# Optimization experiments

Measured on AMD Instinct MI355X. Metric: run time of the kernel, lower is better.

Reference implementation:

```python
import jax, jax.numpy as jnp
import numpy as np

B, C_IN, T = 32, 22, 5000
EMB, P = 64, 100
HOP, NFFT, SR = 25, 128, 250
MIN_SZ, MAX_SZ = 10, 100
OC = 40
SCALES = (9, 25, 49)
FC = OC * len(SCALES)
_freqs = np.arange(NFFT // 2 + 1) * SR / NFFT
MU_IDX = np.nonzero((_freqs >= 8) & (_freqs <= 13))[0]   # bins 5,6
BETA_IDX = np.nonzero((_freqs >= 13) & (_freqs <= 30))[0]  # bins 7..15


def setup_inputs() -> dict:
    key = jax.random.key(0)
    k = iter(jax.random.split(key, 16))
    inp = {"x": jax.random.normal(next(k), (B, C_IN, T), jnp.float32)}
    for i, s in enumerate(SCALES):
        inp[f"ms{i}_w1"] = jax.random.normal(next(k), (OC, 1, 1, s), jnp.float32) * 0.05
        inp[f"ms{i}_b1"] = jnp.zeros((OC,), jnp.float32)
        inp[f"ms{i}_w2"] = jax.random.normal(next(k), (OC, OC, C_IN, 1), jnp.float32) * 0.05
        inp[f"ms{i}_b2"] = jnp.zeros((OC,), jnp.float32)
        inp[f"ms{i}_g"] = jnp.ones((OC,), jnp.float32)
        inp[f"ms{i}_bt"] = jnp.zeros((OC,), jnp.float32)
        inp[f"ms{i}_m"] = jnp.zeros((OC,), jnp.float32)
        inp[f"ms{i}_v"] = jnp.ones((OC,), jnp.float32)
    inp["a_w1"] = jax.random.normal(next(k), (C_IN // 2, C_IN, 3), jnp.float32) * 0.05
    inp["a_b1"] = jnp.zeros((C_IN // 2,), jnp.float32)
    inp["a_g"] = jnp.ones((C_IN // 2,), jnp.float32)
    inp["a_bt"] = jnp.zeros((C_IN // 2,), jnp.float32)
    inp["a_m"] = jnp.zeros((C_IN // 2,), jnp.float32)
    inp["a_v"] = jnp.ones((C_IN // 2,), jnp.float32)
    inp["a_w2"] = jax.random.normal(next(k), (1, C_IN // 2, 1), jnp.float32) * 0.05
    inp["a_b2"] = jnp.zeros((1,), jnp.float32)
    inp["proj_w"] = jax.random.normal(next(k), (EMB, FC, 1), jnp.float32) * 0.05
    inp["proj_b"] = jnp.zeros((EMB,), jnp.float32)
    return inp


def _conv1d(x, w, pad):
    return jax.lax.conv_general_dilated(x, w, (1,), [(pad, pad)],
                                        dimension_numbers=("NCH", "OIH", "NCH"))


def _bn(y, g, bt, m, v):  # eval-mode BatchNorm over channel dim of [B, C, T]
    return (y - m[None, :, None]) * jax.lax.rsqrt(v[None, :, None] + 1e-5) * g[None, :, None] + bt[None, :, None]


def _branch(x, w1, b1, w2, b2, g, bt, m, v):
    # Conv2d(1,OC,(1,ks)) on [B,1,C,T] == per-channel 1D conv over time.
    oc, _, _, ks = w1.shape
    b_, c_, t_ = x.shape
    y = _conv1d(x.reshape(b_ * c_, 1, t_), w1.reshape(oc, 1, ks), (ks - 1) // 2) + b1[None, :, None]
    y = y.reshape(b_, c_, oc, t_).transpose(0, 2, 1, 3)            # [B, OC, C, T]
    # Conv2d(OC,OC,(C,1)) collapses the channel (height) dim.
    y = jnp.einsum("oih,biht->bot", w2[..., 0], y) + b2[None, :, None]
    return jax.nn.elu(_bn(y, g, bt, m, v))                         # [B, OC, T]


def _stft_power(x):
    # torchaudio Spectrogram: center=True, reflect pad, periodic hann, power=2
    pad = NFFT // 2
    xp = jnp.pad(x, ((0, 0), (0, 0), (pad, pad)), mode="reflect")
    nfr = T // HOP  # module truncates to t // hop frames
    idx = jnp.arange(nfr)[:, None] * HOP + jnp.arange(NFFT)[None, :]
    win = 0.5 * (1.0 - jnp.cos(2.0 * jnp.pi * jnp.arange(NFFT) / NFFT))
    frames = xp[..., idx] * win                                    # [B, C, nfr, NFFT]
    spec = jnp.fft.rfft(frames, axis=-1)
    return spec.real ** 2 + spec.imag ** 2                         # [B, C, nfr, NFFT//2+1]


def _interp_linear(a, n):  # F.interpolate(mode='linear', align_corners=False) on [B, L]
    L = a.shape[-1]
    pos = jnp.clip((jnp.arange(n) + 0.5) * (L / n) - 0.5, 0.0, L - 1.0)
    lo = jnp.floor(pos).astype(jnp.int32)
    hi = jnp.minimum(lo + 1, L - 1)
    w = pos - lo
    return a[:, lo] * (1.0 - w) + a[:, hi] * w


def _adaptive_grid(act):
    w = 1.0 / (act + 1e-6)
    w = w / jnp.sum(w, axis=1, keepdims=True)
    gs = jnp.clip(w * T, MIN_SZ, MAX_SZ)
    gs = gs * (T / jnp.sum(gs, axis=1, keepdims=True))
    gsr = jnp.round(gs).astype(jnp.int32)
    gsr = gsr.at[:, -1].add(T - jnp.sum(gsr, axis=1))
    gsf = jnp.clip(gsr, MIN_SZ, MAX_SZ)
    gsf = gsf.at[:, -1].add(T - jnp.sum(gsf, axis=1))
    return jnp.where(gsf < MIN_SZ, MIN_SZ, gsf)


def _forward(x, ms0_w1, ms0_b1, ms0_w2, ms0_b2, ms0_g, ms0_bt, ms0_m, ms0_v,
             ms1_w1, ms1_b1, ms1_w2, ms1_b2, ms1_g, ms1_bt, ms1_m, ms1_v,
             ms2_w1, ms2_b1, ms2_w2, ms2_b2, ms2_g, ms2_bt, ms2_m, ms2_v,
             a_w1, a_b1, a_g, a_bt, a_m, a_v, a_w2, a_b2, proj_w, proj_b):
    # ---- frequency-domain activity detector ----
    spec = _stft_power(x)                                          # [B, C, 200, F]
    comb = spec[..., MU_IDX].mean(-1) + spec[..., BETA_IDX].mean(-1)  # [B, C, 200]
    a = jax.nn.relu(_bn(_conv1d(comb, a_w1, 1) + a_b1[None, :, None], a_g, a_bt, a_m, a_v))
    a = jnp.einsum("oi,bit->bot", a_w2[..., 0], a)[:, 0] + a_b2[0]
    activity = jax.nn.sigmoid(a)                                   # [B, 200]
    act_i = _interp_linear(activity, P)                            # [B, P]
    grid = _adaptive_grid(act_i)                                   # [B, P] int32, sums ~= T
    ends = jnp.cumsum(grid, axis=1)
    starts = ends - grid
    # ---- multi-scale CNN features ----
    feats = jnp.concatenate([
        _branch(x, ms0_w1, ms0_b1, ms0_w2, ms0_b2, ms0_g, ms0_bt, ms0_m, ms0_v),
        _branch(x, ms1_w1, ms1_b1, ms1_w2, ms1_b2, ms1_g, ms1_bt, ms1_m, ms1_v),
        _branch(x, ms2_w1, ms2_b1, ms2_w2, ms2_b2, ms2_g, ms2_bt, ms2_m, ms2_v)],
        axis=1)                                                    # [B, FC, T]
    # ---- ragged per-patch avg+max pooling via segment reductions ----
    tix = jnp.arange(T)
    seg = jax.vmap(lambda e: jnp.searchsorted(e, tix, side="right"))(ends)  # [B,T] in [0,P]
    flat = (seg + jnp.arange(B)[:, None] * (P + 1)).reshape(-1)
    f = feats.transpose(0, 2, 1).reshape(B * T, FC)
    nseg = B * (P + 1)  # extra slot collects any overflow timesteps
    sums = jax.ops.segment_sum(f, flat, num_segments=nseg)
    cnt = jax.ops.segment_sum(jnp.ones((B * T, 1), f.dtype), flat, num_segments=nseg)
    mx = jax.ops.segment_max(f, flat, num_segments=nseg)
    avg = sums / jnp.maximum(cnt, 1.0)
    mx = jnp.where(cnt > 0, mx, 0.0)
    pooled = (avg + mx).reshape(B, P + 1, FC)[:, :P]               # combined avg+max
    valid = ((ends <= T) & (starts < ends))[..., None]
    pooled = jnp.where(valid, pooled, 0.0)
    emb = jnp.einsum("oc,bpc->bpo", proj_w[..., 0], pooled) + proj_b  # [B, P, EMB]
    return emb, grid, act_i


def reference(x, ms0_w1, ms0_b1, ms0_w2, ms0_b2, ms0_g, ms0_bt, ms0_m, ms0_v,
              ms1_w1, ms1_b1, ms1_w2, ms1_b2, ms1_g, ms1_bt, ms1_m, ms1_v,
              ms2_w1, ms2_b1, ms2_w2, ms2_b2, ms2_g, ms2_bt, ms2_m, ms2_v,
              a_w1, a_b1, a_g, a_bt, a_m, a_v, a_w2, a_b2, proj_w, proj_b):
    return _forward(x, ms0_w1, ms0_b1, ms0_w2, ms0_b2, ms0_g, ms0_bt, ms0_m, ms0_v,
                    ms1_w1, ms1_b1, ms1_w2, ms1_b2, ms1_g, ms1_bt, ms1_m, ms1_v,
                    ms2_w1, ms2_b1, ms2_w2, ms2_b2, ms2_g, ms2_bt, ms2_m, ms2_v,
                    a_w1, a_b1, a_g, a_bt, a_m, a_v, a_w2, a_b2, proj_w, proj_b)
```

## Files before the change

kernel.cpp:

```cpp
#include <hip/hip_runtime.h>
#include <hip/hip_bf16.h>
#include <hip/hip_fp8.h>
#include <math.h>
#include <string.h>

#define B 32
#define CIN 22
#define T 5000
#define EMB 64
#define P 100
#define HOP 25
#define OC 40
#define FC 120
#define NBIN 11
#define NFR 200

#define TCH 256
#define CROWS 304
#define RS8 40

#define XPAD 5128
#define TWROW 24

typedef __attribute__((ext_vector_type(4))) float f32x4;

__device__ __forceinline__ unsigned short f2bf(float f) {
  unsigned u = __float_as_uint(f);
  unsigned r = (u + 0x7FFFu + ((u >> 16) & 1u)) >> 16;
  return (unsigned short)r;
}
__device__ __forceinline__ float bf2f(unsigned short u) {
  return __uint_as_float(((unsigned)u) << 16);
}
__device__ __forceinline__ unsigned char f2fp8(float f) {
  __hip_fp8_e4m3 q(f);
  return (unsigned char)q.__x;
}
__device__ __forceinline__ float fast_elu(float y) {
  return y > 0.f ? y : (__builtin_amdgcn_exp2f(y * 1.44269504088896340736f) - 1.0f);
}
__device__ __forceinline__ unsigned pack2bf(float a, float b) {
  __hip_bfloat162 h = __float22bfloat162_rn(make_float2(a, b));
  unsigned u;
  memcpy(&u, &h, 4);
  return u;
}
__device__ __forceinline__ float wave_sum_f(float v) {
  #pragma unroll
  for (int off = 1; off < 64; off <<= 1) v += __shfl_xor(v, off);
  return v;
}
__device__ __forceinline__ int wave_sum_i(int v) {
  #pragma unroll
  for (int off = 1; off < 64; off <<= 1) v += __shfl_xor(v, off);
  return v;
}

struct SetupArgs {
  const float* w1[3]; const float* b1[3]; const float* w2[3]; const float* b2[3];
  const float* g[3];  const float* bt[3]; const float* m[3];  const float* v[3];
  unsigned char* pw8;
  float* A; float* Bc; float* tw;
};

__global__ __launch_bounds__(256) void setup_all(SetupArgs args) {
  int bx = blockIdx.x;
  int tid = threadIdx.x;
  if (bx < 63) {
    int id = bx * 256 + tid;
    if (id < 15936) {
      int fi = id >> 6;
      int lane = id & 63;
      int s, KS, fl;
      if (fi < 27)       { s = 0; KS = 9;  fl = fi; }
      else if (fi < 102) { s = 1; KS = 25; fl = fi - 27; }
      else               { s = 2; KS = 49; fl = fi - 102; }
      int k = fl / 3, ot = fl - k * 3;
      int m = lane & 15, hb = (lane >> 4) << 3;
      int o = ot * 16 + m;
      float val[8];
      #pragma unroll
      for (int j = 0; j < 8; ++j) val[j] = 0.f;
      if (o < OC && hb < CIN) {
        const float* w1 = args.w1[s];
        const float* w2 = args.w2[s];
        if (hb + 8 <= CIN) {
          for (int i = 0; i < OC; ++i) {
            float wv = w1[i * KS + k];
            const float* w2r = w2 + (size_t)(o * OC + i) * CIN + hb;
            float2 a0 = *(const float2*)(w2r + 0);
            float2 a1 = *(const float2*)(w2r + 2);
            float2 a2 = *(const float2*)(w2r + 4);
            float2 a3 = *(const float2*)(w2r + 6);
            val[0] = fmaf(a0.x, wv, val[0]); val[1] = fmaf(a0.y, wv, val[1]);
            val[2] = fmaf(a1.x, wv, val[2]); val[3] = fmaf(a1.y, wv, val[3]);
            val[4] = fmaf(a2.x, wv, val[4]); val[5] = fmaf(a2.y, wv, val[5]);
            val[6] = fmaf(a3.x, wv, val[6]); val[7] = fmaf(a3.y, wv, val[7]);
          }
        } else {
          for (int i = 0; i < OC; ++i) {
            float wv = w1[i * KS + k];
            const float* w2r = w2 + (size_t)(o * OC + i) * CIN + hb;
            float2 a0 = *(const float2*)(w2r + 0);
            float2 a1 = *(const float2*)(w2r + 2);
            float2 a2 = *(const float2*)(w2r + 4);
            val[0] = fmaf(a0.x, wv, val[0]); val[1] = fmaf(a0.y, wv, val[1]);
            val[2] = fmaf(a1.x, wv, val[2]); val[3] = fmaf(a1.y, wv, val[3]);
            val[4] = fmaf(a2.x, wv, val[4]); val[5] = fmaf(a2.y, wv, val[5]);
          }
        }
      }
      unsigned char bytes[8];
      #pragma unroll
      for (int j = 0; j < 8; ++j) bytes[j] = f2fp8(val[j]);
      long long pk;
      memcpy(&pk, bytes, 8);
      *(long long*)(args.pw8 + (size_t)fi * 512 + lane * 8) = pk;
    }
  } else if (bx < 69) {
    int id = (bx - 63) * 256 + tid;
    if (id < 1408) {
      int n = id & 127, k = id >> 7;
      const double PI = 3.14159265358979323846;
      double ang = -2.0 * PI * (double)((k + 5) * n) / 128.0;
      double win = 0.5 * (1.0 - cos(2.0 * PI * (double)n / 128.0));
      args.tw[n * TWROW + 2 * k]     = (float)(cos(ang) * win);
      args.tw[n * TWROW + 2 * k + 1] = (float)(sin(ang) * win);
    } else if (id < 1536) {
      int n = id - 1408;
      args.tw[n * TWROW + 22] = 0.f;
      args.tw[n * TWROW + 23] = 0.f;
    }
  } else {
    if (tid < 120) {
      int s = tid / 40, o = tid - s * 40;
      const float* w2 = args.w2[s];
      float sc = args.g[s][o] / sqrtf(args.v[s][o] + 1e-5f);
      float cc = args.b2[s][o];
      for (int i = 0; i < OC; ++i) {
        float sh = 0.f;
        for (int h = 0; h < CIN; ++h) sh += w2[(o * OC + i) * CIN + h];
        cc = fmaf(args.b1[s][i], sh, cc);
      }
      args.A[tid] = sc;
      args.Bc[tid] = cc * sc + (args.bt[s][o] - args.m[s][o] * sc);
    }
  }
}

__global__ __launch_bounds__(256) void stft_comb(const float* __restrict__ x,
                                                 const float* __restrict__ tw,
                                                 float* __restrict__ comb) {
  __shared__ float xsh[XPAD];
  int bc = blockIdx.x;
  const float* xr = x + (size_t)bc * T;
  int tid = threadIdx.x;
  for (int i = tid; i < XPAD; i += 256) {
    int mm = i - 64;
    mm = (mm < 0) ? -mm : mm;
    mm = (mm >= T) ? (2 * T - 2 - mm) : mm;
    xsh[i] = xr[mm];
  }
  __syncthreads();
  int fr = tid;
  if (fr < NFR) {
    float cr[NBIN], ci[NBIN];
    #pragma unroll
    for (int k = 0; k < NBIN; ++k) { cr[k] = 0.f; ci[k] = 0.f; }
    const float* xw = xsh + fr * HOP;
    #pragma unroll 2
    for (int n = 0; n < 128; ++n) {
      float xv = xw[n];
      const float4* t4 = reinterpret_cast<const float4*>(tw + n * TWROW);
      float4 w0 = t4[0], w1 = t4[1], w2 = t4[2], w3 = t4[3], w4 = t4[4], w5 = t4[5];
      cr[0] = fmaf(xv, w0.x, cr[0]); ci[0] = fmaf(xv, w0.y, ci[0]);
      cr[1] = fmaf(xv, w0.z, cr[1]); ci[1] = fmaf(xv, w0.w, ci[1]);
      cr[2] = fmaf(xv, w1.x, cr[2]); ci[2] = fmaf(xv, w1.y, ci[2]);
      cr[3] = fmaf(xv, w1.z, cr[3]); ci[3] = fmaf(xv, w1.w, ci[3]);
      cr[4] = fmaf(xv, w2.x, cr[4]); ci[4] = fmaf(xv, w2.y, ci[4]);
      cr[5] = fmaf(xv, w2.z, cr[5]); ci[5] = fmaf(xv, w2.w, ci[5]);
      cr[6] = fmaf(xv, w3.x, cr[6]); ci[6] = fmaf(xv, w3.y, ci[6]);
      cr[7] = fmaf(xv, w3.z, cr[7]); ci[7] = fmaf(xv, w3.w, ci[7]);
      cr[8] = fmaf(xv, w4.x, cr[8]); ci[8] = fmaf(xv, w4.y, ci[8]);
      cr[9] = fmaf(xv, w4.z, cr[9]); ci[9] = fmaf(xv, w4.w, ci[9]);
      cr[10] = fmaf(xv, w5.x, cr[10]); ci[10] = fmaf(xv, w5.y, ci[10]);
    }
    float p[NBIN];
    #pragma unroll
    for (int k = 0; k < NBIN; ++k) p[k] = cr[k] * cr[k] + ci[k] * ci[k];
    float beta = 0.f;
    #pragma unroll
    for (int k = 2; k < NBIN; ++k) beta += p[k];
    comb[bc * NFR + fr] = 0.5f * (p[0] + p[1]) + beta * (1.f / 9.f);
  }
}

struct MidSmem {
  union {
    struct {
      float cl[CIN * NFR];
      float actL[NFR];
      float aiL[P];
      float fL[P];
      int giL[P];
      int sI[P];
      float red;
    } a;
    unsigned char xs8[CROWS * RS8];
  };
};

template <int KS, int FB, int SBASE>
__device__ __forceinline__ void scale_body(const unsigned char* __restrict__ xs8,
                                           const unsigned char* __restrict__ pw8,
                                           const float* __restrict__ Aff,
                                           const float* __restrict__ Bff,
                                           unsigned short* __restrict__ feats,
                                           int b, int t0, int wt0, int lane) {
  constexpr int PAD = (KS - 1) / 2;
  const int n = lane & 15, q = lane >> 4;
  f32x4 acc[3][2];
  #pragma unroll
  for (int ot = 0; ot < 3; ++ot)
    #pragma unroll
    for (int ti = 0; ti < 2; ++ti)
      acc[ot][ti] = (f32x4){0.f, 0.f, 0.f, 0.f};

  const unsigned char* pws = pw8 + (size_t)FB * 512 + lane * 8;
  long long A0 = *(const long long*)(pws);
  long long A1 = *(const long long*)(pws + 512);
  long long A2 = *(const long long*)(pws + 1024);
  #pragma unroll 1
  for (int k = 0; k < KS; ++k) {
    long long nA0 = 0, nA1 = 0, nA2 = 0;
    if (k + 1 < KS) {
      const unsigned char* p = pws + (size_t)(k + 1) * 3 * 512;
      nA0 = *(const long long*)(p);
      nA1 = *(const long long*)(p + 512);
      nA2 = *(const long long*)(p + 1024);
    }
    int rbase = 24 - PAD + k + wt0 + n;
    #pragma unroll
    for (int ti = 0; ti < 2; ++ti) {
      long long Bf = *(const long long*)(xs8 + (rbase + ti * 16) * RS8 + q * 8);
      acc[0][ti] = __builtin_amdgcn_mfma_f32_16x16x32_fp8_fp8(A0, Bf, acc[0][ti], 0, 0, 0);
      acc[1][ti] = __builtin_amdgcn_mfma_f32_16x16x32_fp8_fp8(A1, Bf, acc[1][ti], 0, 0, 0);
      acc[2][ti] = __builtin_amdgcn_mfma_f32_16x16x32_fp8_fp8(A2, Bf, acc[2][ti], 0, 0, 0);
    }
    A0 = nA0; A1 = nA1; A2 = nA2;
  }
  #pragma unroll
  for (int ot = 0; ot < 3; ++ot) {
    int obase = ot * 16 + q * 4;
    if (obase < OC) {
      float Av0 = Aff[SBASE + obase + 0], Bv0 = Bff[SBASE + obase + 0];
      float Av1 = Aff[SBASE + obase + 1], Bv1 = Bff[SBASE + obase + 1];
      float Av2 = Aff[SBASE + obase + 2], Bv2 = Bff[SBASE + obase + 2];
      float Av3 = Aff[SBASE + obase + 3], Bv3 = Bff[SBASE + obase + 3];
      #pragma unroll
      for (int ti = 0; ti < 2; ++ti) {
        int tt = t0 + wt0 + ti * 16 + n;
        if (tt < T) {
          uint2 pk;
          pk.x = pack2bf(fast_elu(fmaf(acc[ot][ti][0], Av0, Bv0)),
                         fast_elu(fmaf(acc[ot][ti][1], Av1, Bv1)));
          pk.y = pack2bf(fast_elu(fmaf(acc[ot][ti][2], Av2, Bv2)),
                         fast_elu(fmaf(acc[ot][ti][3], Av3, Bv3)));
          *reinterpret_cast<uint2*>(feats + (size_t)(b * T + tt) * FC + SBASE + obase) = pk;
        }
      }
    }
  }
}

struct MidArgs {
  const float* x;
  const unsigned char* pw8;
  const float* Aff; const float* Bff;
  unsigned short* feats;
  const float* comb;
  const float* aw1; const float* ab1;
  const float* ag;  const float* abt;
  const float* am;  const float* av;
  const float* aw2; const float* ab2;
  float* out_grid; float* out_acti;
  int* ends_i; int* grid_i;
};

__global__ __launch_bounds__(512) void mid_all(MidArgs args) {
  __shared__ MidSmem sm;
  int bx = blockIdx.x;
  int tid = threadIdx.x;
  if (bx >= B) {
    int cx = bx - B;
    int b = cx / 20, t0 = (cx - b * 20) * TCH;
    for (int i = tid; i < CROWS * RS8 / 4; i += 512)
      reinterpret_cast<unsigned*>(sm.xs8)[i] = 0u;
    __syncthreads();
    for (int idx = tid; idx < CIN * CROWS; idx += 512) {
      int h = idx / CROWS, tl = idx - h * CROWS;
      int gt = t0 - 24 + tl;
      float v = (gt >= 0 && gt < T) ? args.x[(size_t)(b * CIN + h) * T + gt] : 0.f;
      sm.xs8[tl * RS8 + h] = f2fp8(v);
    }
    __syncthreads();
    int wv = tid >> 6, lane = tid & 63;
    int wt0 = wv * 32;
    scale_body<9, 0, 0>(sm.xs8, args.pw8, args.Aff, args.Bff, args.feats, b, t0, wt0, lane);
    scale_body<25, 27, 40>(sm.xs8, args.pw8, args.Aff, args.Bff, args.feats, b, t0, wt0, lane);
    scale_body<49, 102, 80>(sm.xs8, args.pw8, args.Aff, args.Bff, args.feats, b, t0, wt0, lane);
  } else {
    int b = bx;
    for (int i = tid; i < CIN * NFR; i += 512) sm.a.cl[i] = args.comb[b * CIN * NFR + i];
    __syncthreads();
    int t = tid;
    if (t < NFR) {
      float z = args.ab2[0];
      for (int o = 0; o < 11; ++o) {
        float s = args.ab1[o];
        for (int i = 0; i < CIN; ++i) {
          const float* wr = args.aw1 + o * 66 + i * 3;
          const float* crow = sm.a.cl + i * NFR;
          if (t > 0)       s = fmaf(wr[0], crow[t - 1], s);
          s = fmaf(wr[1], crow[t], s);
          if (t < NFR - 1) s = fmaf(wr[2], crow[t + 1], s);
        }
        float rs = 1.0f / sqrtf(args.av[o] + 1e-5f);
        float y = (s - args.am[o]) * rs * args.ag[o] + args.abt[o];
        y = fmaxf(y, 0.f);
        z = fmaf(args.aw2[o], y, z);
      }
      sm.a.actL[t] = 1.f / (1.f + expf(-z));
    }
    __syncthreads();
    if (t < P) {
      float ai = 0.5f * (sm.a.actL[2 * t] + sm.a.actL[2 * t + 1]);
      sm.a.aiL[t] = ai;
      args.out_acti[b * P + t] = ai;
      sm.a.fL[t] = 1.f / (ai + 1e-6f);
    }
    __syncthreads();
    if (t < 64) {
      float v = sm.a.fL[t] + ((t + 64 < P) ? sm.a.fL[t + 64] : 0.f);
      v = wave_sum_f(v);
      if (t == 0) sm.a.red = v;
    }
    __syncthreads();
    float sw = sm.a.red;
    if (t < P) {
      float ggv = (sm.a.fL[t] / sw) * 5000.f;
      ggv = fminf(fmaxf(ggv, 10.f), 100.f);
      sm.a.fL[t] = ggv;
    }
    __syncthreads();
    if (t < 64) {
      float v = sm.a.fL[t] + ((t + 64 < P) ? sm.a.fL[t + 64] : 0.f);
      v = wave_sum_f(v);
      if (t == 0) sm.a.red = v;
    }
    __syncthreads();
    float r = 5000.f / sm.a.red;
    if (t < P) sm.a.giL[t] = (int)rintf(sm.a.fL[t] * r);
    __syncthreads();
    if (t < 64) {
      int v = sm.a.giL[t] + ((t + 64 < P) ? sm.a.giL[t + 64] : 0);
      v = wave_sum_i(v);
      if (t == 0) sm.a.red = __int_as_float(v);
    }
    __syncthreads();
    if (t == P - 1) sm.a.giL[P - 1] += 5000 - __float_as_int(sm.a.red);
    __syncthreads();
    if (t < P) sm.a.giL[t] = min(max(sm.a.giL[t], 10), 100);
    __syncthreads();
    if (t < 64) {
      int v = sm.a.giL[t] + ((t + 64 < P) ? sm.a.giL[t + 64] : 0);
      v = wave_sum_i(v);
      if (t == 0) sm.a.red = __int_as_float(v);
    }
    __syncthreads();
    if (t == P - 1) sm.a.giL[P - 1] += 5000 - __float_as_int(sm.a.red);
    __syncthreads();
    if (t < P) sm.a.sI[t] = max(sm.a.giL[t], 10);
    __syncthreads();
    #pragma unroll
    for (int off = 1; off < P; off <<= 1) {
      int v = 0;
      if (t < P && t >= off) v = sm.a.sI[t - off];
      __syncthreads();
      if (t < P) sm.a.sI[t] += v;
      __syncthreads();
    }
    if (t < P) {
      int g2 = max(sm.a.giL[t], 10);
      args.out_grid[b * P + t] = (float)g2;
      args.grid_i[b * P + t] = g2;
      args.ends_i[b * P + t] = sm.a.sI[t];
    }
  }
}

__global__ __launch_bounds__(256) void pool_proj(const unsigned short* __restrict__ feats,
                                                 const int* __restrict__ ends_i,
                                                 const int* __restrict__ grid_i,
                                                 const float* __restrict__ proj_w,
                                                 const float* __restrict__ proj_b,
                                                 float* __restrict__ out_emb) {
  int bp = blockIdx.x;
  int b = bp / P;
  int end = ends_i[bp];
  int gr = grid_i[bp];
  int start = end - gr;
  __shared__ float lds_s[16 * FC];
  __shared__ float lds_m[16 * FC];
  __shared__ float pooled[FC];
  int tid = threadIdx.x;
  bool valid = (end <= T);
  int g = tid % 15;
  int r = tid / 15;
  if (valid && r < 16) {
    float s[8], m[8];
    #pragma unroll
    for (int j = 0; j < 8; ++j) { s[j] = 0.f; m[j] = -INFINITY; }
    const unsigned short* base = feats + (size_t)(b * T + start) * FC + g * 8;
    for (int i = r; i < gr; i += 16) {
      uint4 u4 = *reinterpret_cast<const uint4*>(base + (size_t)i * FC);
      unsigned w[4] = {u4.x, u4.y, u4.z, u4.w};
      #pragma unroll
      for (int j = 0; j < 4; ++j) {
        float v0 = bf2f((unsigned short)(w[j] & 0xffffu));
        float v1 = bf2f((unsigned short)(w[j] >> 16));
        s[2 * j] += v0; s[2 * j + 1] += v1;
        m[2 * j] = fmaxf(m[2 * j], v0); m[2 * j + 1] = fmaxf(m[2 * j + 1], v1);
      }
    }
    #pragma unroll
    for (int j = 0; j < 8; ++j) {
      lds_s[r * FC + g * 8 + j] = s[j];
      lds_m[r * FC + g * 8 + j] = m[j];
    }
  }
  __syncthreads();
  if (tid < FC) {
    if (valid) {
      float s = 0.f, mx = -INFINITY;
      #pragma unroll
      for (int rr = 0; rr < 16; ++rr) {
        s += lds_s[rr * FC + tid];
        mx = fmaxf(mx, lds_m[rr * FC + tid]);
      }
      pooled[tid] = s / (float)gr + mx;
    } else {
      pooled[tid] = 0.f;
    }
  }
  __syncthreads();
  if (tid < EMB) {
    float e = proj_b[tid];
    const float* wr = proj_w + tid * FC;
    #pragma unroll 8
    for (int c = 0; c < FC; ++c) e = fmaf(wr[c], pooled[c], e);
    out_emb[(size_t)bp * EMB + tid] = e;
  }
}

extern "C" void kernel_launch(void* const* d_in, const int* in_sizes, int n_in,
                              void* d_out, int out_size, void* d_ws, size_t ws_size,
                              hipStream_t stream) {
  const float* x = (const float*)d_in[0];
  const float* aw1 = (const float*)d_in[25];
  const float* ab1 = (const float*)d_in[26];
  const float* ag  = (const float*)d_in[27];
  const float* abt = (const float*)d_in[28];
  const float* am  = (const float*)d_in[29];
  const float* av  = (const float*)d_in[30];
  const float* aw2 = (const float*)d_in[31];
  const float* ab2 = (const float*)d_in[32];
  const float* proj_w = (const float*)d_in[33];
  const float* proj_b = (const float*)d_in[34];

  float* wsf = (float*)d_ws;
  float* A    = wsf;
  float* Bc   = wsf + 120;
  float* tw   = wsf + 240;
  float* comb = wsf + 4096;
  int* ends_i = (int*)(wsf + 144896);
  int* grid_i = (int*)(wsf + 148096);
  unsigned char* pw8 = (unsigned char*)(wsf + 151296);
  unsigned short* feats = (unsigned short*)(wsf + 215040);

  float* out      = (float*)d_out;
  float* out_emb  = out;
  float* out_grid = out + 204800;
  float* out_acti = out + 208000;

  SetupArgs sa;
  MidArgs ma;
  for (int s = 0; s < 3; ++s) {
    sa.w1[s] = (const float*)d_in[1 + 8 * s];
    sa.b1[s] = (const float*)d_in[2 + 8 * s];
    sa.w2[s] = (const float*)d_in[3 + 8 * s];
    sa.b2[s] = (const float*)d_in[4 + 8 * s];
    sa.g[s]  = (const float*)d_in[5 + 8 * s];
    sa.bt[s] = (const float*)d_in[6 + 8 * s];
    sa.m[s]  = (const float*)d_in[7 + 8 * s];
    sa.v[s]  = (const float*)d_in[8 + 8 * s];
  }
  sa.pw8 = pw8; sa.A = A; sa.Bc = Bc; sa.tw = tw;

  ma.x = x; ma.pw8 = pw8; ma.Aff = A; ma.Bff = Bc; ma.feats = feats;
  ma.comb = comb; ma.aw1 = aw1; ma.ab1 = ab1; ma.ag = ag; ma.abt = abt;
  ma.am = am; ma.av = av; ma.aw2 = aw2; ma.ab2 = ab2;
  ma.out_grid = out_grid; ma.out_acti = out_acti;
  ma.ends_i = ends_i; ma.grid_i = grid_i;

  setup_all<<<70, 256, 0, stream>>>(sa);
  stft_comb<<<B * CIN, 256, 0, stream>>>(x, tw, comb);
  mid_all<<<B + 20 * B, 512, 0, stream>>>(ma);
  pool_proj<<<B * P, 256, 0, stream>>>(feats, ends_i, grid_i, proj_w, proj_b, out_emb);
}
```

Before: 262.8 us.

## Widen per-wave time tile to 64 rows and prefetch B fragments in conv MFMA loop

Each wave now accumulates four 16-row time tiles instead of two, and the block shrinks from 512 to 256 threads so a block still covers 256 time steps. Each weight fragment loaded from global memory is therefore reused across twice as many MFMAs. The shared-memory B fragments are also software-prefetched one tap ahead, and the loop is unrolled by two with a peeled final iteration. The cost is more accumulator registers and half as many threads for the shared-memory staging and the attention branch of the same kernel.

```diff
diff --git a/kernel.cpp b/kernel.cpp
--- a/kernel.cpp
+++ b/kernel.cpp
@@ -219,36 +219,61 @@
                                            int b, int t0, int wt0, int lane) {
   constexpr int PAD = (KS - 1) / 2;
   const int n = lane & 15, q = lane >> 4;
-  f32x4 acc[3][2];
+  f32x4 acc[3][4];
   #pragma unroll
   for (int ot = 0; ot < 3; ++ot)
     #pragma unroll
-    for (int ti = 0; ti < 2; ++ti)
+    for (int ti = 0; ti < 4; ++ti)
       acc[ot][ti] = (f32x4){0.f, 0.f, 0.f, 0.f};
 
   const unsigned char* pws = pw8 + (size_t)FB * 512 + lane * 8;
+  const unsigned char* xrow = xs8 + (24 - PAD + wt0 + n) * RS8 + q * 8;
   long long A0 = *(const long long*)(pws);
   long long A1 = *(const long long*)(pws + 512);
   long long A2 = *(const long long*)(pws + 1024);
-  #pragma unroll 1
-  for (int k = 0; k < KS; ++k) {
-    long long nA0 = 0, nA1 = 0, nA2 = 0;
-    if (k + 1 < KS) {
-      const unsigned char* p = pws + (size_t)(k + 1) * 3 * 512;
-      nA0 = *(const long long*)(p);
-      nA1 = *(const long long*)(p + 512);
-      nA2 = *(const long long*)(p + 1024);
-    }
-    int rbase = 24 - PAD + k + wt0 + n;
-    #pragma unroll
-    for (int ti = 0; ti < 2; ++ti) {
-      long long Bf = *(const long long*)(xs8 + (rbase + ti * 16) * RS8 + q * 8);
-      acc[0][ti] = __builtin_amdgcn_mfma_f32_16x16x32_fp8_fp8(A0, Bf, acc[0][ti], 0, 0, 0);
-      acc[1][ti] = __builtin_amdgcn_mfma_f32_16x16x32_fp8_fp8(A1, Bf, acc[1][ti], 0, 0, 0);
-      acc[2][ti] = __builtin_amdgcn_mfma_f32_16x16x32_fp8_fp8(A2, Bf, acc[2][ti], 0, 0, 0);
-    }
+  long long B0 = *(const long long*)(xrow);
+  long long B1 = *(const long long*)(xrow + 16 * RS8);
+  long long B2 = *(const long long*)(xrow + 32 * RS8);
+  long long B3 = *(const long long*)(xrow + 48 * RS8);
+  #pragma unroll 2
+  for (int k = 0; k < KS - 1; ++k) {
+    const unsigned char* p = pws + (size_t)(k + 1) * 1536;
+    long long nA0 = *(const long long*)(p);
+    long long nA1 = *(const long long*)(p + 512);
+    long long nA2 = *(const long long*)(p + 1024);
+    const unsigned char* xr = xrow + (k + 1) * RS8;
+    long long nB0 = *(const long long*)(xr);
+    long long nB1 = *(const long long*)(xr + 16 * RS8);
+    long long nB2 = *(const long long*)(xr + 32 * RS8);
+    long long nB3 = *(const long long*)(xr + 48 * RS8);
+    acc[0][0] = __builtin_amdgcn_mfma_f32_16x16x32_fp8_fp8(A0, B0, acc[0][0], 0, 0, 0);
+    acc[1][0] = __builtin_amdgcn_mfma_f32_16x16x32_fp8_fp8(A1, B0, acc[1][0], 0, 0, 0);
+    acc[2][0] = __builtin_amdgcn_mfma_f32_16x16x32_fp8_fp8(A2, B0, acc[2][0], 0, 0, 0);
+    acc[0][1] = __builtin_amdgcn_mfma_f32_16x16x32_fp8_fp8(A0, B1, acc[0][1], 0, 0, 0);
+    acc[1][1] = __builtin_amdgcn_mfma_f32_16x16x32_fp8_fp8(A1, B1, acc[1][1], 0, 0, 0);
+    acc[2][1] = __builtin_amdgcn_mfma_f32_16x16x32_fp8_fp8(A2, B1, acc[2][1], 0, 0, 0);
+    acc[0][2] = __builtin_amdgcn_mfma_f32_16x16x32_fp8_fp8(A0, B2, acc[0][2], 0, 0, 0);
+    acc[1][2] = __builtin_amdgcn_mfma_f32_16x16x32_fp8_fp8(A1, B2, acc[1][2], 0, 0, 0);
+    acc[2][2] = __builtin_amdgcn_mfma_f32_16x16x32_fp8_fp8(A2, B2, acc[2][2], 0, 0, 0);
+    acc[0][3] = __builtin_amdgcn_mfma_f32_16x16x32_fp8_fp8(A0, B3, acc[0][3], 0, 0, 0);
+    acc[1][3] = __builtin_amdgcn_mfma_f32_16x16x32_fp8_fp8(A1, B3, acc[1][3], 0, 0, 0);
+    acc[2][3] = __builtin_amdgcn_mfma_f32_16x16x32_fp8_fp8(A2, B3, acc[2][3], 0, 0, 0);
     A0 = nA0; A1 = nA1; A2 = nA2;
-  }
+    B0 = nB0; B1 = nB1; B2 = nB2; B3 = nB3;
+  }
+  acc[0][0] = __builtin_amdgcn_mfma_f32_16x16x32_fp8_fp8(A0, B0, acc[0][0], 0, 0, 0);
+  acc[1][0] = __builtin_amdgcn_mfma_f32_16x16x32_fp8_fp8(A1, B0, acc[1][0], 0, 0, 0);
+  acc[2][0] = __builtin_amdgcn_mfma_f32_16x16x32_fp8_fp8(A2, B0, acc[2][0], 0, 0, 0);
+  acc[0][1] = __builtin_amdgcn_mfma_f32_16x16x32_fp8_fp8(A0, B1, acc[0][1], 0, 0, 0);
+  acc[1][1] = __builtin_amdgcn_mfma_f32_16x16x32_fp8_fp8(A1, B1, acc[1][1], 0, 0, 0);
+  acc[2][1] = __builtin_amdgcn_mfma_f32_16x16x32_fp8_fp8(A2, B1, acc[2][1], 0, 0, 0);
+  acc[0][2] = __builtin_amdgcn_mfma_f32_16x16x32_fp8_fp8(A0, B2, acc[0][2], 0, 0, 0);
+  acc[1][2] = __builtin_amdgcn_mfma_f32_16x16x32_fp8_fp8(A1, B2, acc[1][2], 0, 0, 0);
+  acc[2][2] = __builtin_amdgcn_mfma_f32_16x16x32_fp8_fp8(A2, B2, acc[2][2], 0, 0, 0);
+  acc[0][3] = __builtin_amdgcn_mfma_f32_16x16x32_fp8_fp8(A0, B3, acc[0][3], 0, 0, 0);
+  acc[1][3] = __builtin_amdgcn_mfma_f32_16x16x32_fp8_fp8(A1, B3, acc[1][3], 0, 0, 0);
+  acc[2][3] = __builtin_amdgcn_mfma_f32_16x16x32_fp8_fp8(A2, B3, acc[2][3], 0, 0, 0);
+
   #pragma unroll
   for (int ot = 0; ot < 3; ++ot) {
     int obase = ot * 16 + q * 4;
@@ -258,7 +283,7 @@
       float Av2 = Aff[SBASE + obase + 2], Bv2 = Bff[SBASE + obase + 2];
       float Av3 = Aff[SBASE + obase + 3], Bv3 = Bff[SBASE + obase + 3];
       #pragma unroll
-      for (int ti = 0; ti < 2; ++ti) {
+      for (int ti = 0; ti < 4; ++ti) {
         int tt = t0 + wt0 + ti * 16 + n;
         if (tt < T) {
           uint2 pk;
@@ -287,17 +312,17 @@
   int* ends_i; int* grid_i;
 };
 
-__global__ __launch_bounds__(512) void mid_all(MidArgs args) {
+__global__ __launch_bounds__(256) void mid_all(MidArgs args) {
   __shared__ MidSmem sm;
   int bx = blockIdx.x;
   int tid = threadIdx.x;
   if (bx >= B) {
     int cx = bx - B;
     int b = cx / 20, t0 = (cx - b * 20) * TCH;
-    for (int i = tid; i < CROWS * RS8 / 4; i += 512)
+    for (int i = tid; i < CROWS * RS8 / 4; i += 256)
       reinterpret_cast<unsigned*>(sm.xs8)[i] = 0u;
     __syncthreads();
-    for (int idx = tid; idx < CIN * CROWS; idx += 512) {
+    for (int idx = tid; idx < CIN * CROWS; idx += 256) {
       int h = idx / CROWS, tl = idx - h * CROWS;
       int gt = t0 - 24 + tl;
       float v = (gt >= 0 && gt < T) ? args.x[(size_t)(b * CIN + h) * T + gt] : 0.f;
@@ -305,13 +330,13 @@
     }
     __syncthreads();
     int wv = tid >> 6, lane = tid & 63;
-    int wt0 = wv * 32;
+    int wt0 = wv * 64;
     scale_body<9, 0, 0>(sm.xs8, args.pw8, args.Aff, args.Bff, args.feats, b, t0, wt0, lane);
     scale_body<25, 27, 40>(sm.xs8, args.pw8, args.Aff, args.Bff, args.feats, b, t0, wt0, lane);
     scale_body<49, 102, 80>(sm.xs8, args.pw8, args.Aff, args.Bff, args.feats, b, t0, wt0, lane);
   } else {
     int b = bx;
-    for (int i = tid; i < CIN * NFR; i += 512) sm.a.cl[i] = args.comb[b * CIN * NFR + i];
+    for (int i = tid; i < CIN * NFR; i += 256) sm.a.cl[i] = args.comb[b * CIN * NFR + i];
     __syncthreads();
     int t = tid;
     if (t < NFR) {
@@ -515,6 +540,6 @@
 
   setup_all<<<70, 256, 0, stream>>>(sa);
   stft_comb<<<B * CIN, 256, 0, stream>>>(x, tw, comb);
-  mid_all<<<B + 20 * B, 512, 0, stream>>>(ma);
+  mid_all<<<B + 20 * B, 256, 0, stream>>>(ma);
   pool_proj<<<B * P, 256, 0, stream>>>(feats, ends_i, grid_i, proj_w, proj_b, out_emb);
 }
```

Result: faster. 257.5 us (-2.0%).
